# Kernel optimization log

Measured on AMD Instinct MI355X. Metric: run time of the kernel, lower is better.

The kernel has to match this reference:

```python
import jax, jax.numpy as jnp
import numpy as np


def _make_cameras(key, B):
    """Well-conditioned c = [cam2world(16), intrinsics(9)] per batch."""
    k1, k2 = jax.random.split(key)
    # random rotation via Gram-Schmidt on a random 3x3
    A = jax.random.normal(k1, (B, 3, 3), dtype=jnp.float32)
    q0 = A[:, :, 0] / jnp.linalg.norm(A[:, :, 0], axis=-1, keepdims=True)
    v1 = A[:, :, 1] - jnp.sum(A[:, :, 1] * q0, -1, keepdims=True) * q0
    q1 = v1 / jnp.linalg.norm(v1, axis=-1, keepdims=True)
    q2 = jnp.cross(q0, q1)
    R = jnp.stack([q0, q1, q2], axis=-1)                      # [B,3,3]
    t = 2.7 * q2                                              # camera at radius 2.7 along view axis
    cam2world = jnp.zeros((B, 4, 4), jnp.float32)
    cam2world = cam2world.at[:, :3, :3].set(R)
    cam2world = cam2world.at[:, :3, 3].set(t)
    cam2world = cam2world.at[:, 3, 3].set(1.0)
    # EG3D-style normalized intrinsics: fx=fy=4.2647, cx=cy=0.5, sk=0
    intr = jnp.tile(jnp.array([[4.2647, 0.0, 0.5],
                               [0.0, 4.2647, 0.5],
                               [0.0, 0.0, 1.0]], jnp.float32), (B, 1, 1))
    return jnp.concatenate([cam2world.reshape(B, 16), intr.reshape(B, 9)], axis=1)


def setup_inputs() -> dict:
    key = jax.random.key(0)
    kc, kd, kp = jax.random.split(key, 3)
    B, R, M = 8, 64, 4096
    c = _make_cameras(kc, B)
    image_depth = 2.2 + 1.1 * jax.random.uniform(kd, (B, R * R, 1), dtype=jnp.float32)
    pc = 0.3 * jax.random.normal(kp, (B, M, 3), dtype=jnp.float32)
    return {"c": c, "image_depth": image_depth, "pc": pc, "resolution": R}


def _ray_sampler(cam2world, intrinsics, resolution):
    B = cam2world.shape[0]
    N = resolution * resolution
    fx = intrinsics[:, 0, 0][:, None]
    fy = intrinsics[:, 1, 1][:, None]
    cx = intrinsics[:, 0, 2][:, None]
    cy = intrinsics[:, 1, 2][:, None]
    sk = intrinsics[:, 0, 1][:, None]
    r = (jnp.arange(resolution, dtype=jnp.float32) + 0.5) / resolution
    gi, gj = jnp.meshgrid(r, r, indexing='ij')                # row, col
    x_cam = jnp.broadcast_to(gj.reshape(-1), (B, N))          # uv.flip(0): x is col coord
    y_cam = jnp.broadcast_to(gi.reshape(-1), (B, N))
    z_cam = jnp.ones((B, N), jnp.float32)
    x_lift = (x_cam - cx + cy * sk / fy - sk * y_cam / fy) / fx * z_cam
    y_lift = (y_cam - cy) / fy * z_cam
    cam_rel = jnp.stack([x_lift, y_lift, z_cam, jnp.ones_like(z_cam)], axis=-1)  # [B,N,4]
    world = jnp.einsum('bij,bnj->bni', cam2world, cam_rel)[..., :3]
    origins = cam2world[:, :3, 3]                              # [B,3]
    dirs = world - origins[:, None, :]
    dirs = dirs / jnp.linalg.norm(dirs, axis=-1, keepdims=True)
    ray_origins = jnp.broadcast_to(origins[:, None, :], dirs.shape)
    return ray_origins, dirs


def _chamfer(x, y):
    # squared-distance NN both directions; GEMM-form pairwise distances
    x2 = jnp.sum(x * x, axis=-1)                               # [B,N]
    y2 = jnp.sum(y * y, axis=-1)                               # [B,M]
    xy = jnp.einsum('bnd,bmd->bnm', x, y)                      # [B,N,M]
    d = x2[:, :, None] + y2[:, None, :] - 2.0 * xy
    return jnp.min(d, axis=2), jnp.min(d, axis=1)              # dist1 [B,N], dist2 [B,M]


def reference(c, image_depth, pc, resolution):
    B = c.shape[0]
    pc = pc[..., :3]
    depth = image_depth.reshape(B, -1, 1)
    cam2world = c[:, :16].reshape(-1, 4, 4)
    intr = c[:, 16:25].reshape(-1, 3, 3)
    ro, rd = _ray_sampler(cam2world, intr, resolution)
    pred_pos = depth * rd + ro                                  # [B,N,3]
    d0, d1 = _chamfer(pred_pos, pc)
    K = min(pred_pos.shape[1], pc.shape[1]) // 2
    d0s = jnp.sort(d0, axis=1)[:, :K]
    d1s = d0s  # NOTE: faithful to original code (loss_1_sorted is assigned from loss_0_sorted)
    loss0 = jnp.mean(d0s, axis=1)
    loss1 = jnp.mean(d1s, axis=1)
    return (loss0 + loss1).reshape(B, 1)
```

## Files before the change

### kernel.cpp

```cpp
#include <hip/hip_runtime.h>
#include <math.h>

#define FLT_BIG 3.0e38f
#define HIST_BINS 16384

typedef short short8 __attribute__((ext_vector_type(8)));
typedef float floatx4 __attribute__((ext_vector_type(4)));

union U4S8 { uint4 u; short8 s; };

static __device__ __forceinline__ unsigned int f2bf(float f) {
    unsigned int u = __float_as_uint(f);
    return (u + 0x7FFFu + ((u >> 16) & 1u)) >> 16;
}
static __device__ __forceinline__ float bf2f(unsigned int b) {
    return __uint_as_float(b << 16);
}

__global__ __launch_bounds__(256, 2) void chamfer_mfma_kernel(
    const float* __restrict__ cparam,
    const float* __restrict__ depth,
    const float* __restrict__ pc,
    float* __restrict__ d0,
    int N, int M, int R)
{
    const int b    = blockIdx.y;
    const int tid  = threadIdx.x;
    const int lane = tid & 63;
    const int wave = tid >> 6;
    const int m16  = lane & 15;
    const int quad = lane >> 4;

    extern __shared__ uint4 sld[];

    const float* pcb = pc + (size_t)b * M * 3;
    const int Ms = M >> 8;
    for (int s = 0; s < Ms; s++) {
        const int idx = s * 256 + tid;
        const float x = pcb[idx * 3 + 0];
        const float y = pcb[idx * 3 + 1];
        const float z = pcb[idx * 3 + 2];
        const float hq = 0.5f * (x * x + y * y + z * z);
        uint4 u;
        u.x = f2bf(x) | (f2bf(y) << 16);
        u.y = f2bf(z) | (f2bf(hq) << 16);
        u.z = 0x3F803F80u;
        u.w = 0u;
        sld[idx] = u;
    }
    __syncthreads();

    const float* cb = cparam + (size_t)b * 25;
    const float fx = cb[16], sk = cb[17], cx = cb[18];
    const float fy = cb[20], cy = cb[21];

    const int nbase = blockIdx.x * 64 + wave * 16;
    const int n  = nbase + m16;
    const int i0 = n / R;
    const int j0 = n - i0 * R;
    const float x_cam = (j0 + 0.5f) / (float)R;
    const float y_cam = (i0 + 0.5f) / (float)R;
    const float x_lift = (x_cam - cx + cy * sk / fy - sk * y_cam / fy) / fx;
    const float y_lift = (y_cam - cy) / fy;
    const float dxw = cb[0] * x_lift + cb[1] * y_lift + cb[2];
    const float dyw = cb[4] * x_lift + cb[5] * y_lift + cb[6];
    const float dzw = cb[8] * x_lift + cb[9] * y_lift + cb[10];
    const float inv = 1.0f / sqrtf(dxw * dxw + dyw * dyw + dzw * dzw);
    const float dep = depth[(size_t)b * N + n];
    const float px = cb[3]  + dep * dxw * inv;
    const float py = cb[7]  + dep * dyw * inv;
    const float pz = cb[11] + dep * dzw * inv;

    const float hp = 0.5f * (px * px + py * py + pz * pz);
    const unsigned int hp_hi = f2bf(hp);
    const unsigned int hp_lo = f2bf(hp - bf2f(hp_hi));

    U4S8 af;
    af.u = make_uint4(0u, 0u, 0u, 0u);
    if (quad == 0) {
        af.u.x = f2bf(-px) | (f2bf(-py) << 16);
        af.u.y = f2bf(-pz) | (0x3F80u << 16);
        af.u.z = hp_hi | (hp_lo << 16);
        af.u.w = 0u;
    }
    const short8 afrag = af.s;
    const floatx4 zero4 = {0.0f, 0.0f, 0.0f, 0.0f};

    floatx4 mins = {FLT_BIG, FLT_BIG, FLT_BIG, FLT_BIG};

    const int T = M >> 4;
    for (int m = 0; m < T; m += 8) {
        uint4 bu[8];
        #pragma unroll
        for (int mm = 0; mm < 8; mm++)
            bu[mm] = sld[((m + mm) << 4) + m16];
        #pragma unroll
        for (int mm = 0; mm < 8; mm++) {
            U4S8 bf; bf.u = bu[mm];
            floatx4 d = __builtin_amdgcn_mfma_f32_16x16x32_bf16(
                            afrag, bf.s, zero4, 0, 0, 0);
            mins[0] = fminf(mins[0], d[0]);
            mins[1] = fminf(mins[1], d[1]);
            mins[2] = fminf(mins[2], d[2]);
            mins[3] = fminf(mins[3], d[3]);
        }
    }

    float dv[4];
    #pragma unroll
    for (int t = 0; t < 4; t++) {
        float v = mins[t];
        v = fminf(v, __shfl_xor(v, 1));
        v = fminf(v, __shfl_xor(v, 2));
        v = fminf(v, __shfl_xor(v, 4));
        v = fminf(v, __shfl_xor(v, 8));
        dv[t] = fmaxf(2.0f * v, 0.0f);
    }
    if (m16 == 0) {
        float4* o = (float4*)(d0 + (size_t)b * N + nbase + quad * 4);
        *o = make_float4(dv[0], dv[1], dv[2], dv[3]);
    }
}

__global__ __launch_bounds__(256, 1) void select_mean_kernel(
    const float* __restrict__ d0,
    float* __restrict__ out,
    int N, int K)
{
    const int b   = blockIdx.x;
    const int tid = threadIdx.x;

    extern __shared__ unsigned int hist[];
    __shared__ unsigned int spart[256];
    __shared__ unsigned int s_selbin, s_krem;
    __shared__ unsigned int subcnt[32];
    __shared__ float        subsum[32];
    __shared__ float        s_below;

    for (int t2 = tid; t2 < HIST_BINS; t2 += 256) hist[t2] = 0u;
    if (tid < 32) { subcnt[tid] = 0u; subsum[tid] = 0.0f; }
    if (tid == 0) s_below = 0.0f;
    __syncthreads();

    unsigned int key[16];
    #pragma unroll
    for (int t2 = 0; t2 < 16; t2++)
        key[t2] = __float_as_uint(d0[(size_t)b * N + t2 * 256 + tid]);
    #pragma unroll
    for (int t2 = 0; t2 < 16; t2++)
        atomicAdd(&hist[key[t2] >> 18], 1u);
    __syncthreads();

    unsigned int psum = 0u;
    #pragma unroll 8
    for (int i2 = 0; i2 < 64; i2++)
        psum += hist[(tid << 6) + ((i2 + tid) & 63)];
    spart[tid] = psum;
    __syncthreads();

    unsigned int cbef = 0u;
    for (int i2 = 0; i2 < tid; i2++) cbef += spart[i2];
    if (cbef < (unsigned int)K && (unsigned int)K <= cbef + psum) {
        unsigned int k2 = (unsigned int)K - cbef;
        unsigned int sel = 0u;
        for (int i2 = 0; i2 < 64; i2++) {
            unsigned int h = hist[(tid << 6) + i2];
            if (k2 <= h) { sel = (tid << 6) + i2; break; }
            k2 -= h;
        }
        s_selbin = sel;
        s_krem   = k2;
    }
    __syncthreads();

    const unsigned int selbin = s_selbin;
    float sumb = 0.0f;
    #pragma unroll
    for (int t2 = 0; t2 < 16; t2++) {
        const unsigned int bin = key[t2] >> 18;
        const float v = __uint_as_float(key[t2]);
        if (bin < selbin) sumb += v;
        if (bin == selbin) {
            const unsigned int sub = (key[t2] >> 13) & 31u;
            atomicAdd(&subcnt[sub], 1u);
            atomicAdd(&subsum[sub], v);
        }
    }
    atomicAdd(&s_below, sumb);
    __syncthreads();

    if (tid == 0) {
        unsigned int k2 = s_krem;
        float s = s_below;
        for (int i2 = 0; i2 < 32; i2++) {
            unsigned int h = subcnt[i2];
            if (k2 <= h) {
                s += (h ? (subsum[i2] * ((float)k2 / (float)h)) : 0.0f);
                break;
            }
            s += subsum[i2];
            k2 -= h;
        }
        out[b] = 2.0f * s / (float)K;
    }
}

extern "C" void kernel_launch(void* const* d_in, const int* in_sizes, int n_in,
                              void* d_out, int out_size, void* d_ws, size_t ws_size,
                              hipStream_t stream)
{
    const float* c   = (const float*)d_in[0];
    const float* dep = (const float*)d_in[1];
    const float* pc  = (const float*)d_in[2];
    float* out = (float*)d_out;

    const int B = in_sizes[0] / 25;
    const int N = in_sizes[1] / B;
    const int M = in_sizes[2] / (3 * B);
    int R = 1; while (R * R < N) R++;

    float* d0 = (float*)d_ws;

    dim3 gridA(N / 64, B);
    size_t ldsA = (size_t)M * sizeof(uint4);
    hipLaunchKernelGGL(chamfer_mfma_kernel, gridA, dim3(256), ldsA, stream,
                       c, dep, pc, d0, N, M, R);

    const int K = ((N < M) ? N : M) / 2;
    size_t ldsB = (size_t)HIST_BINS * sizeof(unsigned int);
    hipLaunchKernelGGL(select_mean_kernel, dim3(B), dim3(256), ldsB, stream,
                       d0, out, N, K);
}
```

Measured before the change: 81.85 us.

## Switch chamfer distance MFMA from 16x16x32 to 32x32x16 with split-M waves

Replaces the 16x16x32 bf16 MFMA with the 32x32x16 variant. Each wave now covers 32 rays against half of the point cloud, and the two halves are merged through a small LDS reduction. This wastes less of the MFMA K dimension on zero padding and halves the number of matrix ops per ray, cutting matrix-core time. In exchange it adds an LDS exchange plus a block barrier, and the loop now hardcodes 64 fragments per half, which implicitly assumes M=4096.

```diff
diff --git a/kernel.cpp b/kernel.cpp
--- a/kernel.cpp
+++ b/kernel.cpp
@@ -6,6 +6,7 @@
 
 typedef short short8 __attribute__((ext_vector_type(8)));
 typedef float floatx4 __attribute__((ext_vector_type(4)));
+typedef float floatx16 __attribute__((ext_vector_type(16)));
 
 union U4S8 { uint4 u; short8 s; };
 
@@ -27,11 +28,12 @@
     const int b    = blockIdx.y;
     const int tid  = threadIdx.x;
     const int lane = tid & 63;
-    const int wave = tid >> 6;
-    const int m16  = lane & 15;
-    const int quad = lane >> 4;
+    const int wv   = tid >> 6;
+    const int row  = lane & 31;
+    const int half = lane >> 5;
 
     extern __shared__ uint4 sld[];
+    __shared__ float smin[4][32];
 
     const float* pcb = pc + (size_t)b * M * 3;
     const int Ms = M >> 8;
@@ -54,8 +56,8 @@
     const float fx = cb[16], sk = cb[17], cx = cb[18];
     const float fy = cb[20], cy = cb[21];
 
-    const int nbase = blockIdx.x * 64 + wave * 16;
-    const int n  = nbase + m16;
+    const int nbase = blockIdx.x * 64;
+    const int n  = nbase + (wv & 1) * 32 + row;
     const int i0 = n / R;
     const int j0 = n - i0 * R;
     const float x_cam = (j0 + 0.5f) / (float)R;
@@ -77,48 +79,61 @@
 
     U4S8 af;
     af.u = make_uint4(0u, 0u, 0u, 0u);
-    if (quad == 0) {
+    if (half == 0) {
         af.u.x = f2bf(-px) | (f2bf(-py) << 16);
         af.u.y = f2bf(-pz) | (0x3F80u << 16);
         af.u.z = hp_hi | (hp_lo << 16);
-        af.u.w = 0u;
     }
     const short8 afrag = af.s;
-    const floatx4 zero4 = {0.0f, 0.0f, 0.0f, 0.0f};
-
-    floatx4 mins = {FLT_BIG, FLT_BIG, FLT_BIG, FLT_BIG};
-
-    const int T = M >> 4;
-    for (int m = 0; m < T; m += 8) {
+    const floatx16 zero16 = {0,0,0,0,0,0,0,0,0,0,0,0,0,0,0,0};
+
+    float minsA[16], minsB[16];
+    #pragma unroll
+    for (int t = 0; t < 16; t++) { minsA[t] = FLT_BIG; minsB[t] = FLT_BIG; }
+
+    const int fbase = (wv >> 1) * 64;
+    for (int f = 0; f < 64; f += 8) {
         uint4 bu[8];
         #pragma unroll
         for (int mm = 0; mm < 8; mm++)
-            bu[mm] = sld[((m + mm) << 4) + m16];
+            bu[mm] = sld[((fbase + f + mm) << 5) + row];
         #pragma unroll
         for (int mm = 0; mm < 8; mm++) {
             U4S8 bf; bf.u = bu[mm];
-            floatx4 d = __builtin_amdgcn_mfma_f32_16x16x32_bf16(
-                            afrag, bf.s, zero4, 0, 0, 0);
-            mins[0] = fminf(mins[0], d[0]);
-            mins[1] = fminf(mins[1], d[1]);
-            mins[2] = fminf(mins[2], d[2]);
-            mins[3] = fminf(mins[3], d[3]);
-        }
-    }
-
-    float dv[4];
-    #pragma unroll
-    for (int t = 0; t < 4; t++) {
-        float v = mins[t];
+            floatx16 d = __builtin_amdgcn_mfma_f32_32x32x16_bf16(
+                             afrag, bf.s, zero16, 0, 0, 0);
+            if (mm & 1) {
+                #pragma unroll
+                for (int t = 0; t < 16; t++) minsB[t] = fminf(minsB[t], d[t]);
+            } else {
+                #pragma unroll
+                for (int t = 0; t < 16; t++) minsA[t] = fminf(minsA[t], d[t]);
+            }
+        }
+    }
+
+    #pragma unroll
+    for (int t = 0; t < 16; t++) {
+        float v = fminf(minsA[t], minsB[t]);
         v = fminf(v, __shfl_xor(v, 1));
         v = fminf(v, __shfl_xor(v, 2));
         v = fminf(v, __shfl_xor(v, 4));
         v = fminf(v, __shfl_xor(v, 8));
-        dv[t] = fmaxf(2.0f * v, 0.0f);
-    }
-    if (m16 == 0) {
-        float4* o = (float4*)(d0 + (size_t)b * N + nbase + quad * 4);
-        *o = make_float4(dv[0], dv[1], dv[2], dv[3]);
+        v = fminf(v, __shfl_xor(v, 16));
+        minsA[t] = v;
+    }
+    if (row == 0) {
+        #pragma unroll
+        for (int t = 0; t < 16; t++)
+            smin[wv][(t & 3) + 8 * (t >> 2) + 4 * half] = minsA[t];
+    }
+    __syncthreads();
+
+    if (tid < 64) {
+        const int g  = tid >> 5;
+        const int rr = tid & 31;
+        const float v = fminf(smin[g][rr], smin[g + 2][rr]);
+        d0[(size_t)b * N + nbase + tid] = fmaxf(2.0f * v, 0.0f);
     }
 }
 
```

New measurement: 80.72 us. No clear change (-1.4%).
